# Performance work log

Measured on AMD Instinct MI355X. Metric: run time of the kernel, lower is better.

Reference implementation:

```python
import jax, jax.numpy as jnp
from jax import lax
import numpy as np

GRIDS = [40, 36, 24, 16, 12]
STRIDES = [4, 8, 16, 32, 64]
SCORE_THR = 0.3
MASK_THR = 0.5
UPDATE_THR = 0.05
SIGMA = 2.0
NMS_PRE = 500
MAX_PER_IMG = 30
E = 128            # ins_out_channels -> kernel_out_channels
HF = WF = 128      # seg feature map; upsampled_size_out = 4*HF = 512
IMG_H = IMG_W = 512
ORI_H = ORI_W = 512

# per-candidate stride, matching the cumsum-based fill in get_seg_single
STRIDE_PER_CELL = np.repeat(np.array(STRIDES, np.float32), [g * g for g in GRIDS])  # [3872]


def setup_inputs() -> dict:
    key = jax.random.key(0)
    ks = jax.random.split(key, 11)
    d = {}
    for i, g in enumerate(GRIDS):
        d[f"cate{i}"] = jax.random.uniform(ks[i], (1, g, g, 1), jnp.float32)
        d[f"kern{i}"] = jax.random.normal(ks[5 + i], (1, E, g, g), jnp.float32)
    d["seg_pred"] = jax.random.normal(ks[10], (1, E, HF, WF), jnp.float32)
    return d


def _forward_scores_and_masks(cates, kerns, seg_pred):
    # flatten all FPN levels, exactly mirroring view(-1,C)/permute(1,2,0).view(-1,E)
    scores = jnp.concatenate([c[0].reshape(-1) for c in cates])                 # [M]
    kernels = jnp.concatenate([k[0].transpose(1, 2, 0).reshape(-1, E) for k in kerns])  # [M,E]
    strides = jnp.asarray(STRIDE_PER_CELL)
    valid = scores > SCORE_THR                                                  # score_thr filter (as mask)

    # dynamic 1x1 conv over mask features == channel contraction
    seg_preds = jax.nn.sigmoid(jnp.einsum('me,ehw->mhw', kernels, seg_pred[0]))  # [M,HF,WF]
    seg_masks = seg_preds > MASK_THR
    sum_masks = seg_masks.sum((1, 2)).astype(jnp.float32)
    keep = valid & (sum_masks > strides)
    seg_scores = (seg_preds * seg_masks).sum((1, 2)) / jnp.maximum(sum_masks, 1.0)
    cscores = jnp.where(keep, scores * seg_scores, 0.0)

    # descending sort + truncate to nms_pre (dropped candidates carry score 0)
    top_scores, top_idx = lax.top_k(cscores, NMS_PRE)
    masks_k = seg_masks[top_idx].reshape(NMS_PRE, -1).astype(jnp.float32)       # [N,HW]
    sm = sum_masks[top_idx]

    # matrix NMS (single foreground class -> label matrix = triu of ones)
    inter = masks_k @ masks_k.T                                                 # [N,N]
    union = sm[None, :] + sm[:, None] - inter
    iou = jnp.triu(inter / jnp.maximum(union, 1.0), k=1)
    comp = iou.max(0)                              # max IoU with any higher-scored mask
    decay = jnp.exp(-SIGMA * (iou ** 2 - comp[:, None] ** 2))
    decay_coeff = decay.min(0)
    nms_scores = top_scores * decay_coeff
    nms_scores = jnp.where(nms_scores >= UPDATE_THR, nms_scores, 0.0)           # update_thr filter

    final_scores, fidx = lax.top_k(nms_scores, MAX_PER_IMG)
    sel = top_idx[fidx]
    sel_preds = seg_preds[sel]                                                  # [K,HF,WF]
    up = jax.image.resize(sel_preds, (MAX_PER_IMG, HF * 4, WF * 4), 'bilinear')  # align_corners=False
    up = up[:, :IMG_H, :IMG_W]
    up = jax.image.resize(up, (MAX_PER_IMG, ORI_H, ORI_W), 'bilinear')
    return final_scores, up


def reference(cate0, cate1, cate2, cate3, cate4,
              kern0, kern1, kern2, kern3, kern4, seg_pred):
    cates = [cate0, cate1, cate2, cate3, cate4]
    kerns = [kern0, kern1, kern2, kern3, kern4]
    final_scores, up = _forward_scores_and_masks(cates, kerns, seg_pred)
    seg_label = up > MASK_THR                                                   # [K,H,W]
    vis = final_scores > SCORE_THR                                              # vis_inds in forward()

    # masks_to_boxes, vectorized; invalid/empty rows zeroed (fixed-size output)
    any_x = seg_label.any(1)                                                    # [K,W]
    any_y = seg_label.any(2)                                                    # [K,H]
    xs = jnp.arange(ORI_W)
    ys = jnp.arange(ORI_H)
    xmin = jnp.min(jnp.where(any_x, xs, ORI_W), axis=1)
    xmax = jnp.max(jnp.where(any_x, xs, -1), axis=1)
    ymin = jnp.min(jnp.where(any_y, ys, ORI_H), axis=1)
    ymax = jnp.max(jnp.where(any_y, ys, -1), axis=1)
    boxes = jnp.stack([xmin, ymin, xmax, ymax], -1).astype(jnp.float32)         # [K,4]
    boxes = jnp.where(vis[:, None], boxes, 0.0)
    return boxes, final_scores, vis.astype(jnp.float32)
```

## Files before the change

kernel.cpp:

```cpp
#include <hip/hip_runtime.h>
#include <math.h>

#define M_CELLS 3872
#define M_PAD   3968
#define NPIX    16384

typedef _Float16 half8 __attribute__((ext_vector_type(8)));
typedef float f32x4 __attribute__((ext_vector_type(4)));

#define GL2LDS(g, l) __builtin_amdgcn_global_load_lds( \
    (const __attribute__((address_space(1))) unsigned int*)(g), \
    (__attribute__((address_space(3))) unsigned int*)(l), 16, 0, 0)

static constexpr size_t ALN(size_t x){ return (x + 255) & ~(size_t)255; }

static constexpr size_t F_KF   = 0;
static constexpr size_t F_SC   = F_KF + (size_t)M_CELLS*128*4;
static constexpr size_t F_SM   = F_SC + (size_t)M_CELLS*4;
static constexpr size_t F_CS   = F_SM + (size_t)M_CELLS*4;
static constexpr size_t F_BIT  = F_CS + (size_t)M_CELLS*4;
static constexpr size_t F_SPP  = F_BIT + (size_t)M_CELLS*256*8;
static constexpr size_t F_TIDX = F_SPP + (size_t)64*M_CELLS*4;
static constexpr size_t F_TSC  = F_TIDX + 512*4;
static constexpr size_t F_SMT  = F_TSC + 512*4;
static constexpr size_t F_IOU  = F_SMT + 512*4;
static constexpr size_t F_COMP = F_IOU + (size_t)500*500*4;
static constexpr size_t F_NMS  = F_COMP + 512*4;
static constexpr size_t F_SEL  = F_NMS + 512*4;
static constexpr size_t F_SELP = F_SEL + 32*4;
static constexpr size_t F_RMN  = ALN(F_SELP + (size_t)30*NPIX*4);
static constexpr size_t F_RMX  = F_RMN + 30*512*4;
static constexpr size_t F_KEYS = ALN(F_RMX + 30*512*4);
static constexpr size_t WS_FB  = F_KEYS + 4096*8;

static constexpr size_t B_KF   = 0;
static constexpr size_t B_AFR  = ALN(B_KF  + (size_t)M_PAD*128*4);
static constexpr size_t B_BFR  = ALN(B_AFR + (size_t)31*4096*16);
static constexpr size_t B_SC   = ALN(B_BFR + (size_t)128*4096*16);
static constexpr size_t B_SM   = ALN(B_SC + (size_t)M_PAD*4);
static constexpr size_t B_CS   = ALN(B_SM + (size_t)M_PAD*4);
static constexpr size_t B_BIT  = ALN(B_CS + (size_t)M_PAD*4);
static constexpr size_t B_SPP  = ALN(B_BIT + (size_t)M_PAD*256*8);
static constexpr size_t B_TIDX = ALN(B_SPP + (size_t)128*M_PAD*4);
static constexpr size_t B_TSC  = ALN(B_TIDX + 512*4);
static constexpr size_t B_SMT  = ALN(B_TSC + 512*4);
static constexpr size_t B_IOU  = ALN(B_SMT + 512*4);
static constexpr size_t B_COMP = ALN(B_IOU + (size_t)500*500*4);
static constexpr size_t B_NMS  = ALN(B_COMP + 512*4);
static constexpr size_t B_SEL  = ALN(B_NMS + 512*4);
static constexpr size_t B_SELP = ALN(B_SEL + 32*4);
static constexpr size_t B_RMN  = ALN(B_SELP + (size_t)30*NPIX*4);
static constexpr size_t B_RMX  = B_RMN + 30*512*4;
static constexpr size_t B_CMAP = ALN(B_RMX + 30*512*4);
static constexpr size_t B_RMAP = B_CMAP + 4096*4;
static constexpr size_t B_VCNT = B_RMAP + 4096*4;
static constexpr size_t B_KEYS = ALN(B_VCNT + 64*4);
static constexpr size_t B_AF30 = ALN(B_KEYS + 4096*8);
static constexpr size_t WS_MFMA = B_AF30 + 8*128*16;

__global__ __launch_bounds__(256) void k0aT_gather(
    const float* __restrict__ c0,const float* __restrict__ c1,const float* __restrict__ c2,
    const float* __restrict__ c3,const float* __restrict__ c4,
    const float* __restrict__ w0,const float* __restrict__ w1,const float* __restrict__ w2,
    const float* __restrict__ w3,const float* __restrict__ w4,
    float* __restrict__ kfT, float* __restrict__ scores,
    int* __restrict__ cmap, int* __restrict__ rmap, int* __restrict__ vcnt) {
  const int lvl = blockIdx.y;
  const int Gs[5]   = {1600,1296,576,256,144};
  const int offs[5] = {0,1600,2896,3472,3728};
  const int G = Gs[lvl], off = offs[lvl];
  const float* kl = (lvl==0)?w0:(lvl==1)?w1:(lvl==2)?w2:(lvl==3)?w3:w4;
  const float* cl = (lvl==0)?c0:(lvl==1)?c1:(lvl==2)?c2:(lvl==3)?c3:c4;
  int t = blockIdx.x*256 + threadIdx.x;
  if (t >= G*128) return;
  int e = t / G, c = t - e*G;
  kfT[(size_t)e*M_PAD + off + c] = kl[t];
  if (e == 0) {
    int cell = off + c;
    float sc = cl[c];
    scores[cell] = sc;
    if (sc > 0.3f) {
      int run = atomicAdd(vcnt, 1);
      cmap[run] = cell;
      rmap[cell] = run;
    } else rmap[cell] = -1;
  }
}

__global__ __launch_bounds__(256) void k0a_gather(
    const float* __restrict__ c0,const float* __restrict__ c1,const float* __restrict__ c2,
    const float* __restrict__ c3,const float* __restrict__ c4,
    const float* __restrict__ w0,const float* __restrict__ w1,const float* __restrict__ w2,
    const float* __restrict__ w3,const float* __restrict__ w4,
    float* __restrict__ kf, float* __restrict__ scores) {
  const int lvl = blockIdx.y;
  const int Gs[5]   = {1600,1296,576,256,144};
  const int offs[5] = {0,1600,2896,3472,3728};
  const int G = Gs[lvl], off = offs[lvl];
  const float* kl = (lvl==0)?w0:(lvl==1)?w1:(lvl==2)?w2:(lvl==3)?w3:w4;
  const float* cl = (lvl==0)?c0:(lvl==1)?c1:(lvl==2)?c2:(lvl==3)?c3:c4;
  int t = blockIdx.x*256 + threadIdx.x;
  if (t >= G*128) return;
  int e = t / G, c = t - e*G;
  kf[(size_t)(off+c)*128 + e] = kl[t];
  if (e == 0) scores[off+c] = cl[c];
}

__global__ __launch_bounds__(256) void k0b_afrag(const float* __restrict__ kfT,
                                                 const int* __restrict__ cmap,
                                                 const int* __restrict__ vcnt,
                                                 _Float16* __restrict__ Af) {
  int P = blockIdx.x*256 + threadIdx.x;
  int mblock = P >> 12;
  int r  = P & 4095;
  int sub = r >> 9, pc = r & 511;
  int ks = sub >> 1, h = sub & 1;
  int mn = pc >> 6, ln = pc & 63;
  int mcomp = mblock*128 + mn*16 + (ln & 15);
  int kb = ks*32 + (ln >> 4)*8;
  half8 o;
  if (mcomp < vcnt[0]) {
    const float* src = kfT + cmap[mcomp];
    #pragma unroll
    for (int j=0;j<8;j++) {
      float x = src[(size_t)(kb+j)*M_PAD];
      _Float16 hi = (_Float16)x;
      o[j] = h ? (_Float16)(x - (float)hi) : hi;
    }
  } else {
    #pragma unroll
    for (int j=0;j<8;j++) o[j] = (_Float16)0.f;
  }
  *(half8*)&Af[(size_t)P*8] = o;
}

__global__ __launch_bounds__(256) void k0c_bfrag(const float* __restrict__ seg,
                                                 _Float16* __restrict__ Bf) {
  int P = blockIdx.x*256 + threadIdx.x;
  int nb = P >> 12;
  int r  = P & 4095;
  int sub = r >> 9, pc = r & 511;
  int ks = sub >> 1, h = sub & 1;
  int mn = pc >> 6, ln = pc & 63;
  int px = nb*128 + mn*16 + (ln & 15);
  int kb = ks*32 + (ln >> 4)*8;
  half8 o;
  #pragma unroll
  for (int j=0;j<8;j++) {
    float x = seg[(size_t)(kb+j)*NPIX + px];
    _Float16 hi = (_Float16)x;
    o[j] = h ? (_Float16)(x - (float)hi) : hi;
  }
  *(half8*)&Bf[(size_t)P*8] = o;
}

__global__ __launch_bounds__(256, 6) void k1_gemm(
    const float* __restrict__ kf, const float* __restrict__ seg,
    unsigned long long* __restrict__ bits, float* __restrict__ spp) {
  int tid = threadIdx.x;
  int p  = blockIdx.x*256 + tid;
  int c0 = blockIdx.y*32;
  float acc[32];
  #pragma unroll
  for (int c=0;c<32;c++) acc[c]=0.f;
  for (int ch=0; ch<8; ch++) {
    float s[16];
    #pragma unroll
    for (int e=0;e<16;e++) s[e] = seg[(size_t)(ch*16+e)*NPIX + p];
    #pragma unroll
    for (int c=0;c<32;c++) {
      float a=0.f;
      #pragma unroll
      for (int e=0;e<16;e++) a = fmaf(kf[(size_t)(c0+c)*128 + ch*16 + e], s[e], a);
      acc[c] += a;
    }
  }
  int wv = tid>>6, ln = tid&63;
  __shared__ float wsum[32][4];
  #pragma unroll
  for (int c=0;c<32;c++) {
    float logit = acc[c];
    bool msk = logit > 0.f;
    unsigned long long bal = __ballot(msk);
    float pr = msk ? __fdividef(1.f, 1.f + __expf(-logit)) : 0.f;
    #pragma unroll
    for (int o=32;o>0;o>>=1) pr += __shfl_down(pr, o);
    if (ln==0) {
      bits[(size_t)(c0+c)*256 + blockIdx.x*4 + wv] = bal;
      wsum[c][wv] = pr;
    }
  }
  __syncthreads();
  if (tid < 32)
    spp[(size_t)blockIdx.x*M_CELLS + c0 + tid] = wsum[tid][0]+wsum[tid][1]+wsum[tid][2]+wsum[tid][3];
}

__global__ __launch_bounds__(256, 4) void k1_mfma(
    const _Float16* __restrict__ Af, const _Float16* __restrict__ Bf,
    const int* __restrict__ vcnt,
    unsigned long long* __restrict__ bits, float* __restrict__ spp) {
  if (blockIdx.x*128 >= vcnt[0]) return;
  __shared__ char lds[32768];
  const int tid  = threadIdx.x;
  const int lane = tid & 63;
  const int wave = tid >> 6;
  const int wr = wave >> 1, wc = wave & 1;
  const char* gA = (const char*)Af + (size_t)blockIdx.x*65536;
  const char* gB = (const char*)Bf + (size_t)blockIdx.y*65536;

  f32x4 acc[4][4];
  #pragma unroll
  for (int a=0;a<4;a++)
    #pragma unroll
    for (int b=0;b<4;b++) acc[a][b] = (f32x4){0.f,0.f,0.f,0.f};

  auto issue = [&](int sub, int buf) {
    const char* ga = gA + sub*8192;
    const char* gb = gB + sub*8192;
    char* la = &lds[buf*16384];
    char* lb = &lds[buf*16384 + 8192];
    GL2LDS(ga +  wave   *1024 + lane*16, la +  wave   *1024);
    GL2LDS(ga + (wave+4)*1024 + lane*16, la + (wave+4)*1024);
    GL2LDS(gb +  wave   *1024 + lane*16, lb +  wave   *1024);
    GL2LDS(gb + (wave+4)*1024 + lane*16, lb + (wave+4)*1024);
  };

  issue(0, 0);
  half8 ah[4], bh[4];
  #pragma unroll
  for (int s=0; s<8; s++) {
    __syncthreads();
    if (s < 7) issue(s+1, (s+1)&1);
    const char* lb_ = &lds[(s&1)*16384];
    if ((s & 1) == 0) {
      #pragma unroll
      for (int mt=0; mt<4; mt++) ah[mt] = *(const half8*)&lb_[(wr*4+mt)*1024 + lane*16];
      #pragma unroll
      for (int nt=0; nt<4; nt++) bh[nt] = *(const half8*)&lb_[8192 + (wc*4+nt)*1024 + lane*16];
      #pragma unroll
      for (int nt=0; nt<4; nt++)
        #pragma unroll
        for (int mt=0; mt<4; mt++)
          acc[mt][nt] = __builtin_amdgcn_mfma_f32_16x16x32_f16(ah[mt], bh[nt], acc[mt][nt], 0, 0, 0);
    } else {
      #pragma unroll
      for (int nt=0; nt<4; nt++) {
        half8 bl = *(const half8*)&lb_[8192 + (wc*4+nt)*1024 + lane*16];
        #pragma unroll
        for (int mt=0; mt<4; mt++)
          acc[mt][nt] = __builtin_amdgcn_mfma_f32_16x16x32_f16(ah[mt], bl, acc[mt][nt], 0, 0, 0);
      }
      #pragma unroll
      for (int mt=0; mt<4; mt++) {
        half8 al = *(const half8*)&lb_[(wr*4+mt)*1024 + lane*16];
        #pragma unroll
        for (int nt=0; nt<4; nt++)
          acc[mt][nt] = __builtin_amdgcn_mfma_f32_16x16x32_f16(al, bh[nt], acc[mt][nt], 0, 0, 0);
      }
    }
  }
  __syncthreads();

  const int q = lane >> 4, mm = lane & 15;
  const int mbase = blockIdx.x * 128;
  const int wordIdx = blockIdx.y*2 + wc;
  float* ldsf = (float*)lds;
  #pragma unroll
  for (int mt=0; mt<4; mt++) {
    #pragma unroll
    for (int reg=0; reg<4; reg++) {
      unsigned long long bal[4];
      float ps = 0.f;
      #pragma unroll
      for (int nt=0; nt<4; nt++) {
        float lg = acc[mt][nt][reg];
        bal[nt] = __ballot(lg > 0.f);
        if (lg > 0.f) ps += __fdividef(1.f, 1.f + __expf(-lg));
      }
      ps += __shfl_xor(ps, 1); ps += __shfl_xor(ps, 2);
      ps += __shfl_xor(ps, 4); ps += __shfl_xor(ps, 8);
      if (mm == 0) {
        int cl = wr*64 + mt*16 + q*4 + reg;
        unsigned long long wd = 0;
        #pragma unroll
        for (int nt=0; nt<4; nt++)
          wd |= ((bal[nt] >> (q*16)) & 0xFFFFull) << (nt*16);
        bits[(size_t)(mbase + cl)*256 + wordIdx] = wd;
        ldsf[cl*2 + wc] = ps;
      }
    }
  }
  __syncthreads();
  if (tid < 128)
    spp[(size_t)blockIdx.y*M_PAD + mbase + tid] = ldsf[tid*2] + ldsf[tid*2+1];
}

__global__ __launch_bounds__(256) void k2c_cscore(
    const unsigned long long* __restrict__ bits, const float* __restrict__ spp,
    const float* __restrict__ scores, const int* __restrict__ rmap,
    float* __restrict__ summ, float* __restrict__ cs) {
  int cell = blockIdx.x*4 + (threadIdx.x>>6);
  int ln = threadIdx.x & 63;
  int ridx = rmap[cell];
  if (ridx < 0) { if (ln==0) { summ[cell]=0.f; cs[cell]=0.f; } return; }
  const unsigned long long* row = bits + (size_t)ridx*256;
  int cnt = 0;
  #pragma unroll
  for (int k=0;k<4;k++) cnt += __popcll(row[ln + 64*k]);
  float sp = 0.f;
  for (int i=ln; i<128; i+=64) sp += spp[(size_t)i*M_PAD + ridx];
  #pragma unroll
  for (int o=32;o>0;o>>=1) { cnt += __shfl_down(cnt,o); sp += __shfl_down(sp,o); }
  if (ln==0) {
    float smf = (float)cnt;
    float sc = scores[cell];
    float strd = (cell<1600)?4.f:(cell<2896)?8.f:(cell<3472)?16.f:(cell<3728)?32.f:64.f;
    bool keep = (smf > strd);
    float ss = sp / fmaxf(smf, 1.f);
    summ[cell] = smf;
    cs[cell] = keep ? sc*ss : 0.f;
  }
}

__global__ __launch_bounds__(256) void k2_cscore(
    const unsigned long long* __restrict__ bits, const float* __restrict__ spp,
    const float* __restrict__ scores, float* __restrict__ summ, float* __restrict__ cs,
    int nparts, int mp) {
  int cell = blockIdx.x*4 + (threadIdx.x>>6);
  int ln = threadIdx.x & 63;
  const unsigned long long* row = bits + (size_t)cell*256;
  int cnt = 0;
  #pragma unroll
  for (int k=0;k<4;k++) cnt += __popcll(row[ln + 64*k]);
  float sp = 0.f;
  for (int i=ln; i<nparts; i+=64) sp += spp[(size_t)i*mp + cell];
  #pragma unroll
  for (int o=32;o>0;o>>=1) { cnt += __shfl_down(cnt,o); sp += __shfl_down(sp,o); }
  if (ln==0) {
    float smf = (float)cnt;
    float sc = scores[cell];
    float strd = (cell<1600)?4.f:(cell<2896)?8.f:(cell<3472)?16.f:(cell<3728)?32.f:64.f;
    bool keep = (sc > 0.3f) && (smf > strd);
    float ss = sp / fmaxf(smf, 1.f);
    summ[cell] = smf;
    cs[cell] = keep ? sc*ss : 0.f;
  }
}

__device__ inline unsigned long long packkey(float v, int i) {
  return ((unsigned long long)__float_as_uint(v) << 32) | (unsigned)(0xFFFFFFFFu - (unsigned)i);
}

__global__ __launch_bounds__(256) void k3a_sort512(const float* __restrict__ cs,
                                                   unsigned long long* __restrict__ keys) {
  __shared__ unsigned long long key[512];
  int b = blockIdx.x, tid = threadIdx.x;
  for (int i=tid;i<512;i+=256) {
    int gi = b*512 + i;
    key[i] = (gi < M_CELLS) ? packkey(cs[gi], gi) : 0ULL;
  }
  __syncthreads();
  for (int size=2; size<=512; size<<=1) {
    for (int st=size>>1; st>0; st>>=1) {
      for (int i=tid;i<512;i+=256) {
        int pp = i ^ st;
        if (pp > i) {
          unsigned long long a=key[i], bb=key[pp];
          bool desc = (((b*512+i) & size) == 0);
          if (desc ? (a<bb) : (a>bb)) { key[i]=bb; key[pp]=a; }
        }
      }
      __syncthreads();
    }
  }
  for (int i=tid;i<512;i+=256) keys[b*512+i] = key[i];
}

__global__ __launch_bounds__(1024) void k3b_merge(const unsigned long long* __restrict__ keys,
    const float* __restrict__ summ,
    int* __restrict__ tidx, float* __restrict__ tsc, float* __restrict__ smt) {
  __shared__ unsigned long long key[4096];
  int tid = threadIdx.x;
  for (int i=tid;i<4096;i+=1024) key[i] = keys[i];
  __syncthreads();
  for (int size=1024; size<=4096; size<<=1) {
    for (int st=size>>1; st>0; st>>=1) {
      for (int i=tid;i<4096;i+=1024) {
        int pp = i ^ st;
        if (pp > i) {
          unsigned long long a=key[i], b=key[pp];
          bool desc = ((i & size) == 0);
          if (desc ? (a<b) : (a>b)) { key[i]=b; key[pp]=a; }
        }
      }
      __syncthreads();
    }
  }
  if (tid < 512) {
    if (tid < 500) {
      unsigned long long k = key[tid];
      int idx = (int)(0xFFFFFFFFu - (unsigned)(k & 0xFFFFFFFFull));
      tidx[tid] = idx;
      tsc[tid] = __uint_as_float((unsigned)(k>>32));
      smt[tid] = summ[idx];
    } else { tidx[tid]=0; tsc[tid]=0.f; smt[tid]=0.f; }
  }
}

__global__ __launch_bounds__(256) void k4_iou(
    const unsigned long long* __restrict__ bits, const int* __restrict__ tidx,
    const int* __restrict__ rmap, const float* __restrict__ smt, float* __restrict__ iou) {
  int ti = blockIdx.y, tj = blockIdx.x;
  int tid = threadIdx.x;
  int ty = tid>>4, tx = tid&15;
  int i = ti*16+ty, j = tj*16+tx;
  if (ti > tj) { if (i<500 && j<500) iou[i*500+j] = 0.f; return; }
  __shared__ unsigned long long A[16][130];
  __shared__ unsigned long long B[16][130];
  __shared__ float sa[16], sb[16];
  if (tid<16) sa[tid] = (ti*16+tid<500) ? smt[ti*16+tid] : 0.f;
  else if (tid<32) sb[tid-16] = (tj*16+tid-16<500) ? smt[tj*16+tid-16] : 0.f;
  int inter = 0;
  for (int half=0; half<2; half++) {
    __syncthreads();
    for (int t=tid;t<2048;t+=256) {
      int r=t>>7, k=t&127;
      int ii = ti*16+r;
      int jj = tj*16+r;
      int ri = (ii<500) ? (rmap ? max(rmap[tidx[ii]],0) : tidx[ii]) : 0;
      int rj = (jj<500) ? (rmap ? max(rmap[tidx[jj]],0) : tidx[jj]) : 0;
      A[r][k] = (ii<500) ? bits[(size_t)ri*256 + half*128 + k] : 0ULL;
      B[r][k] = (jj<500) ? bits[(size_t)rj*256 + half*128 + k] : 0ULL;
    }
    __syncthreads();
    for (int k=0;k<128;k++) inter += __popcll(A[ty][k] & B[tx][k]);
  }
  if (i<500 && j<500) {
    float fi = (float)inter;
    float un = sa[ty] + sb[tx] - fi;
    iou[i*500+j] = (i<j) ? fi / fmaxf(un, 1.f) : 0.f;
  }
}

__global__ __launch_bounds__(256) void k5_comp(const float* __restrict__ iou, float* __restrict__ comp) {
  int tid = threadIdx.x;
  int tx = tid & 63, ty = tid >> 6;
  int j = blockIdx.x*64 + tx;
  float m0=0.f, m1=0.f, m2=0.f, m3=0.f;
  if (j < 500) {
    int i = ty;
    for (; i+12 < 500; i += 16) {
      m0 = fmaxf(m0, iou[(i   )*500 + j]);
      m1 = fmaxf(m1, iou[(i+ 4)*500 + j]);
      m2 = fmaxf(m2, iou[(i+ 8)*500 + j]);
      m3 = fmaxf(m3, iou[(i+12)*500 + j]);
    }
    for (; i < 500; i += 4) m0 = fmaxf(m0, iou[i*500 + j]);
  }
  float m = fmaxf(fmaxf(m0,m1), fmaxf(m2,m3));
  __shared__ float red[4][64];
  red[ty][tx] = m;
  __syncthreads();
  if (ty == 0 && j < 512)
    comp[j] = (j < 500) ? fmaxf(fmaxf(red[0][tx],red[1][tx]), fmaxf(red[2][tx],red[3][tx])) : 0.f;
}

__global__ __launch_bounds__(256) void k6_decay(
    const float* __restrict__ iou, const float* __restrict__ comp,
    const float* __restrict__ tsc, float* __restrict__ nms) {
  __shared__ float csh[512];
  int tid = threadIdx.x;
  for (int i=tid; i<512; i+=256) csh[i] = (i<500) ? comp[i] : 0.f;
  __syncthreads();
  int tx = tid & 63, ty = tid >> 6;
  int j = blockIdx.x*64 + tx;
  float t0=-1e30f, t1=-1e30f, t2=-1e30f, t3=-1e30f;
  if (j < 500) {
    int i = ty;
    for (; i+12 < 500; i += 16) {
      float v0 = iou[(i   )*500 + j], c0 = csh[i];
      float v1 = iou[(i+ 4)*500 + j], c1 = csh[i+4];
      float v2 = iou[(i+ 8)*500 + j], c2 = csh[i+8];
      float v3 = iou[(i+12)*500 + j], c3 = csh[i+12];
      t0 = fmaxf(t0, v0*v0 - c0*c0);
      t1 = fmaxf(t1, v1*v1 - c1*c1);
      t2 = fmaxf(t2, v2*v2 - c2*c2);
      t3 = fmaxf(t3, v3*v3 - c3*c3);
    }
    for (; i < 500; i += 4) { float v = iou[i*500 + j]; float c = csh[i]; t0 = fmaxf(t0, v*v - c*c); }
  }
  float t = fmaxf(fmaxf(t0,t1), fmaxf(t2,t3));
  __shared__ float red[4][64];
  red[ty][tx] = t;
  __syncthreads();
  if (ty == 0 && j < 512) {
    float out = 0.f;
    if (j < 500) {
      float tt = fmaxf(fmaxf(red[0][tx],red[1][tx]), fmaxf(red[2][tx],red[3][tx]));
      float s = tsc[j] * __expf(-2.f*tt);
      out = (s >= 0.05f) ? s : 0.f;
    }
    nms[j] = out;
  }
}

__global__ __launch_bounds__(256) void k7_top30(
    const float* __restrict__ nms, const int* __restrict__ tidx,
    int* __restrict__ sel, float* __restrict__ out,
    const float* __restrict__ kfT, _Float16* __restrict__ Af30) {
  __shared__ unsigned long long key[512];
  __shared__ int selsh[30];
  int tid = threadIdx.x;
  for (int i=tid;i<512;i+=256) key[i] = (i<500) ? packkey(nms[i], i) : 0ULL;
  __syncthreads();
  for (int size=2; size<=512; size<<=1) {
    for (int st=size>>1; st>0; st>>=1) {
      for (int i=tid;i<512;i+=256) {
        int pp = i ^ st;
        if (pp > i) {
          unsigned long long a=key[i], b=key[pp];
          bool desc = ((i & size) == 0);
          if (desc ? (a<b) : (a>b)) { key[i]=b; key[pp]=a; }
        }
      }
      __syncthreads();
    }
  }
  if (tid < 30) {
    unsigned long long k = key[tid];
    int j = (int)(0xFFFFFFFFu - (unsigned)(k & 0xFFFFFFFFull));
    float v = __uint_as_float((unsigned)(k>>32));
    out[120+tid] = v;
    out[150+tid] = (v > 0.3f) ? 1.f : 0.f;
    sel[tid] = tidx[j];
    selsh[tid] = tidx[j];
  }
  __syncthreads();
  if (kfT) {
    for (int P = tid; P < 1024; P += 256) {
      int sub = P >> 7, pc = P & 127;
      int ks = sub >> 1, h = sub & 1;
      int mn = pc >> 6, ln = pc & 63;
      int m  = mn*16 + (ln & 15);
      int kb = ks*32 + (ln >> 4)*8;
      half8 o;
      if (m < 30) {
        const float* src = kfT + selsh[m];
        #pragma unroll
        for (int j=0;j<8;j++) {
          float x = src[(size_t)(kb+j)*M_PAD];
          _Float16 hi = (_Float16)x;
          o[j] = h ? (_Float16)(x - (float)hi) : hi;
        }
      } else {
        #pragma unroll
        for (int j=0;j<8;j++) o[j] = (_Float16)0.f;
      }
      *(half8*)&Af30[(size_t)P*8] = o;
    }
  }
}

__global__ __launch_bounds__(256) void k8_mfma(const _Float16* __restrict__ Af30,
                                               const _Float16* __restrict__ Bf,
                                               float* __restrict__ selp) {
  const int nb = blockIdx.x;
  const int lane = threadIdx.x & 63;
  const int w = threadIdx.x >> 6;
  const half8* A = (const half8*)Af30;
  const half8* B = (const half8*)Bf + (size_t)nb*4096;
  f32x4 acc[2][2];
  #pragma unroll
  for (int a=0;a<2;a++)
    #pragma unroll
    for (int b=0;b<2;b++) acc[a][b] = (f32x4){0.f,0.f,0.f,0.f};
  #pragma unroll
  for (int ks=0; ks<4; ks++) {
    half8 ah[2], bh[2], al[2], bl[2];
    #pragma unroll
    for (int mt=0; mt<2; mt++) ah[mt] = A[(ks*2+0)*128 + mt*64 + lane];
    #pragma unroll
    for (int nt=0; nt<2; nt++) bh[nt] = B[(size_t)(ks*2+0)*512 + (w*2+nt)*64 + lane];
    #pragma unroll
    for (int mt=0; mt<2; mt++) al[mt] = A[(ks*2+1)*128 + mt*64 + lane];
    #pragma unroll
    for (int nt=0; nt<2; nt++) bl[nt] = B[(size_t)(ks*2+1)*512 + (w*2+nt)*64 + lane];
    #pragma unroll
    for (int nt=0; nt<2; nt++)
      #pragma unroll
      for (int mt=0; mt<2; mt++) {
        acc[mt][nt] = __builtin_amdgcn_mfma_f32_16x16x32_f16(ah[mt], bh[nt], acc[mt][nt], 0, 0, 0);
        acc[mt][nt] = __builtin_amdgcn_mfma_f32_16x16x32_f16(ah[mt], bl[nt], acc[mt][nt], 0, 0, 0);
        acc[mt][nt] = __builtin_amdgcn_mfma_f32_16x16x32_f16(al[mt], bh[nt], acc[mt][nt], 0, 0, 0);
      }
  }
  const int q = lane >> 4, col = lane & 15;
  #pragma unroll
  for (int mt=0; mt<2; mt++)
    #pragma unroll
    for (int nt=0; nt<2; nt++)
      #pragma unroll
      for (int reg=0; reg<4; reg++) {
        int m = mt*16 + q*4 + reg;
        if (m < 30) {
          int px = nb*128 + w*32 + nt*16 + col;
          float lg = acc[mt][nt][reg];
          selp[(size_t)m*NPIX + px] = __fdividef(1.f, 1.f + __expf(-lg));
        }
      }
}

__global__ __launch_bounds__(256) void k8_selp(
    const float* __restrict__ kf, const float* __restrict__ seg,
    const int* __restrict__ sel, float* __restrict__ selp) {
  int px = blockIdx.x*256 + threadIdx.x;
  int cells[30];
  #pragma unroll
  for (int m=0;m<30;m++) cells[m] = __builtin_amdgcn_readfirstlane(sel[m]);
  float acc[30];
  #pragma unroll
  for (int m=0;m<30;m++) acc[m] = 0.f;
  for (int e=0; e<128; e+=4) {
    float s0 = seg[(size_t)(e+0)*NPIX + px];
    float s1 = seg[(size_t)(e+1)*NPIX + px];
    float s2 = seg[(size_t)(e+2)*NPIX + px];
    float s3 = seg[(size_t)(e+3)*NPIX + px];
    #pragma unroll
    for (int m=0;m<30;m++) {
      const float* kr = kf + (size_t)cells[m]*128 + e;
      acc[m] = fmaf(kr[0], s0, fmaf(kr[1], s1, fmaf(kr[2], s2, fmaf(kr[3], s3, acc[m]))));
    }
  }
  #pragma unroll
  for (int m=0;m<30;m++)
    selp[(size_t)m*NPIX + px] = __fdividef(1.f, 1.f + __expf(-acc[m]));
}

__global__ __launch_bounds__(256) void k9a_rows(const float* __restrict__ selp,
                                               int* __restrict__ rowmn, int* __restrict__ rowmx) {
  int msk = blockIdx.y, oy = blockIdx.x;
  const float* mp = selp + (size_t)msk*NPIX;
  __shared__ float rows[2][128];
  __shared__ int wmn[4], wmx[4];
  int tid = threadIdx.x;
  float yf = fminf(fmaxf((oy+0.5f)*0.25f - 0.5f, 0.f), 127.f);
  int y0 = (int)yf, y1 = min(y0+1,127);
  float fy = yf-(float)y0;
  if (tid < 128) rows[0][tid] = mp[y0*128 + tid];
  else           rows[1][tid-128] = mp[y1*128 + tid-128];
  __syncthreads();
  int mnx = 512, mxx = -1;
  #pragma unroll
  for (int h=0; h<2; h++) {
    int ox = tid + h*256;
    float xf = fminf(fmaxf((ox+0.5f)*0.25f - 0.5f, 0.f), 127.f);
    int x0 = (int)xf, x1 = min(x0+1,127);
    float fx = xf-(float)x0;
    float v0 = rows[0][x0]*(1.f-fx) + rows[0][x1]*fx;
    float v1 = rows[1][x0]*(1.f-fx) + rows[1][x1]*fx;
    float v  = v0*(1.f-fy) + v1*fy;
    if (v > 0.5f) { mnx = min(mnx, ox); mxx = max(mxx, ox); }
  }
  #pragma unroll
  for (int o=32;o>0;o>>=1) {
    mnx = min(mnx, __shfl_down(mnx, o));
    mxx = max(mxx, __shfl_down(mxx, o));
  }
  if ((tid & 63) == 0) { wmn[tid>>6] = mnx; wmx[tid>>6] = mxx; }
  __syncthreads();
  if (tid == 0) {
    rowmn[msk*512 + oy] = min(min(wmn[0],wmn[1]), min(wmn[2],wmn[3]));
    rowmx[msk*512 + oy] = max(max(wmx[0],wmx[1]), max(wmx[2],wmx[3]));
  }
}

__global__ __launch_bounds__(512) void k9b_box(const int* __restrict__ rowmn,
                                              const int* __restrict__ rowmx, float* out) {
  int msk = blockIdx.x, tid = threadIdx.x;
  __shared__ int r0[512], r1[512], r2[512], r3[512];
  int mn = rowmn[msk*512 + tid];
  int mx = rowmx[msk*512 + tid];
  bool occ = (mx >= 0);
  r0[tid] = mn;
  r1[tid] = mx;
  r2[tid] = occ ? tid : 512;
  r3[tid] = occ ? tid : -1;
  __syncthreads();
  for (int s=256;s>0;s>>=1) {
    if (tid<s) {
      r0[tid]=min(r0[tid],r0[tid+s]); r1[tid]=max(r1[tid],r1[tid+s]);
      r2[tid]=min(r2[tid],r2[tid+s]); r3[tid]=max(r3[tid],r3[tid+s]);
    }
    __syncthreads();
  }
  if (tid==0) {
    bool vis = out[120+msk] > 0.3f;
    out[msk*4+0] = vis ? (float)r0[0] : 0.f;
    out[msk*4+1] = vis ? (float)r2[0] : 0.f;
    out[msk*4+2] = vis ? (float)r1[0] : 0.f;
    out[msk*4+3] = vis ? (float)r3[0] : 0.f;
  }
}

extern "C" void kernel_launch(void* const* d_in, const int* in_sizes, int n_in,
                              void* d_out, int out_size, void* d_ws, size_t ws_size,
                              hipStream_t stream) {
  (void)in_sizes; (void)n_in; (void)out_size;
  if (ws_size < WS_FB) return;
  const float* cate[5]; const float* kern[5];
  for (int i=0;i<5;i++){ cate[i]=(const float*)d_in[2*i]; kern[i]=(const float*)d_in[2*i+1]; }
  const float* seg = (const float*)d_in[10];
  char* ws = (char*)d_ws;
  float* out = (float*)d_out;

  const bool mfma = (ws_size >= WS_MFMA);

  float* kf      = (float*)(ws + (mfma ? B_KF   : F_KF));
  float* scores  = (float*)(ws + (mfma ? B_SC   : F_SC));
  float* summ    = (float*)(ws + (mfma ? B_SM   : F_SM));
  float* cs      = (float*)(ws + (mfma ? B_CS   : F_CS));
  unsigned long long* bits = (unsigned long long*)(ws + (mfma ? B_BIT : F_BIT));
  float* spp     = (float*)(ws + (mfma ? B_SPP  : F_SPP));
  int*   tidx    = (int*)(ws + (mfma ? B_TIDX : F_TIDX));
  float* tsc     = (float*)(ws + (mfma ? B_TSC  : F_TSC));
  float* smt     = (float*)(ws + (mfma ? B_SMT  : F_SMT));
  float* iou     = (float*)(ws + (mfma ? B_IOU  : F_IOU));
  float* comp    = (float*)(ws + (mfma ? B_COMP : F_COMP));
  float* nms     = (float*)(ws + (mfma ? B_NMS  : F_NMS));
  int*   sel     = (int*)(ws + (mfma ? B_SEL  : F_SEL));
  float* selp    = (float*)(ws + (mfma ? B_SELP : F_SELP));
  int*   rowmn   = (int*)(ws + (mfma ? B_RMN  : F_RMN));
  int*   rowmx   = (int*)(ws + (mfma ? B_RMX  : F_RMX));
  unsigned long long* keys = (unsigned long long*)(ws + (mfma ? B_KEYS : F_KEYS));

  if (mfma) {
    _Float16* Af = (_Float16*)(ws + B_AFR);
    _Float16* Bf = (_Float16*)(ws + B_BFR);
    _Float16* Af30 = (_Float16*)(ws + B_AF30);
    int* cmap = (int*)(ws + B_CMAP);
    int* rmap = (int*)(ws + B_RMAP);
    int* vcnt = (int*)(ws + B_VCNT);
    hipMemsetAsync(vcnt, 0, 4, stream);
    k0aT_gather<<<dim3(800,5), 256, 0, stream>>>(cate[0],cate[1],cate[2],cate[3],cate[4],
                                      kern[0],kern[1],kern[2],kern[3],kern[4],
                                      kf, scores, cmap, rmap, vcnt);
    k0c_bfrag<<<128*4096/256, 256, 0, stream>>>(seg, Bf);
    k0b_afrag<<<31*4096/256, 256, 0, stream>>>(kf, cmap, vcnt, Af);
    k1_mfma  <<<dim3(31, 128), 256, 0, stream>>>(Af, Bf, vcnt, bits, spp);
    k2c_cscore<<<M_CELLS/4, 256, 0, stream>>>(bits, spp, scores, rmap, summ, cs);
    k3a_sort512<<<8, 256, 0, stream>>>(cs, keys);
    k3b_merge  <<<1, 1024, 0, stream>>>(keys, summ, tidx, tsc, smt);
    k4_iou   <<<dim3(32,32), 256, 0, stream>>>(bits, tidx, rmap, smt, iou);
    k5_comp  <<<8, 256, 0, stream>>>(iou, comp);
    k6_decay <<<8, 256, 0, stream>>>(iou, comp, tsc, nms);
    k7_top30 <<<1, 256, 0, stream>>>(nms, tidx, sel, out, kf, Af30);
    k8_mfma  <<<128, 256, 0, stream>>>(Af30, Bf, selp);
  } else {
    k0a_gather<<<dim3(800,5), 256, 0, stream>>>(cate[0],cate[1],cate[2],cate[3],cate[4],
                                      kern[0],kern[1],kern[2],kern[3],kern[4], kf, scores);
    k1_gemm  <<<dim3(64,121), 256, 0, stream>>>(kf, seg, bits, spp);
    k2_cscore<<<M_CELLS/4, 256, 0, stream>>>(bits, spp, scores, summ, cs, 64, M_CELLS);
    k3a_sort512<<<8, 256, 0, stream>>>(cs, keys);
    k3b_merge  <<<1, 1024, 0, stream>>>(keys, summ, tidx, tsc, smt);
    k4_iou   <<<dim3(32,32), 256, 0, stream>>>(bits, tidx, nullptr, smt, iou);
    k5_comp  <<<8, 256, 0, stream>>>(iou, comp);
    k6_decay <<<8, 256, 0, stream>>>(iou, comp, tsc, nms);
    k7_top30 <<<1, 256, 0, stream>>>(nms, tidx, sel, out, nullptr, nullptr);
    k8_selp  <<<NPIX/256, 256, 0, stream>>>(kf, seg, sel, selp);
  }
  k9a_rows <<<dim3(512,30), 256, 0, stream>>>(selp, rowmn, rowmx);
  k9b_box  <<<30, 512, 0, stream>>>(rowmn, rowmx, out);
}
```

Measured before the change: 278.3 us.

## Merge small post-GEMM stages into cooperative kernels with grid-wide syncs

Replaces the cscore, two-pass sort and merge kernels with one cooperative kernel, the comp/decay/top30 kernels with a second, and the two bbox kernels with a third, each using grid.sync between phases. The aim is to cut kernel launch and inter-kernel gap overhead across a chain of tiny kernels. The cost is grid-wide barrier latency, and in coop_bbox some phases now run on a limited number of blocks, which lowers parallelism. Cooperative launch also requires every block to be co-resident on the device.

```diff
diff --git a/kernel.cpp b/kernel.cpp
--- a/kernel.cpp
+++ b/kernel.cpp
@@ -1,5 +1,8 @@
 #include <hip/hip_runtime.h>
+#include <hip/hip_cooperative_groups.h>
 #include <math.h>
+
+namespace cg = cooperative_groups;
 
 #define M_CELLS 3872
 #define M_PAD   3968
@@ -57,6 +60,10 @@
 static constexpr size_t B_KEYS = ALN(B_VCNT + 64*4);
 static constexpr size_t B_AF30 = ALN(B_KEYS + 4096*8);
 static constexpr size_t WS_MFMA = B_AF30 + 8*128*16;
+
+__device__ inline unsigned long long packkey(float v, int i) {
+  return ((unsigned long long)__float_as_uint(v) << 32) | (unsigned)(0xFFFFFFFFu - (unsigned)i);
+}
 
 __global__ __launch_bounds__(256) void k0aT_gather(
     const float* __restrict__ c0,const float* __restrict__ c1,const float* __restrict__ c2,
@@ -295,33 +302,6 @@
     spp[(size_t)blockIdx.y*M_PAD + mbase + tid] = ldsf[tid*2] + ldsf[tid*2+1];
 }
 
-__global__ __launch_bounds__(256) void k2c_cscore(
-    const unsigned long long* __restrict__ bits, const float* __restrict__ spp,
-    const float* __restrict__ scores, const int* __restrict__ rmap,
-    float* __restrict__ summ, float* __restrict__ cs) {
-  int cell = blockIdx.x*4 + (threadIdx.x>>6);
-  int ln = threadIdx.x & 63;
-  int ridx = rmap[cell];
-  if (ridx < 0) { if (ln==0) { summ[cell]=0.f; cs[cell]=0.f; } return; }
-  const unsigned long long* row = bits + (size_t)ridx*256;
-  int cnt = 0;
-  #pragma unroll
-  for (int k=0;k<4;k++) cnt += __popcll(row[ln + 64*k]);
-  float sp = 0.f;
-  for (int i=ln; i<128; i+=64) sp += spp[(size_t)i*M_PAD + ridx];
-  #pragma unroll
-  for (int o=32;o>0;o>>=1) { cnt += __shfl_down(cnt,o); sp += __shfl_down(sp,o); }
-  if (ln==0) {
-    float smf = (float)cnt;
-    float sc = scores[cell];
-    float strd = (cell<1600)?4.f:(cell<2896)?8.f:(cell<3472)?16.f:(cell<3728)?32.f:64.f;
-    bool keep = (smf > strd);
-    float ss = sp / fmaxf(smf, 1.f);
-    summ[cell] = smf;
-    cs[cell] = keep ? sc*ss : 0.f;
-  }
-}
-
 __global__ __launch_bounds__(256) void k2_cscore(
     const unsigned long long* __restrict__ bits, const float* __restrict__ spp,
     const float* __restrict__ scores, float* __restrict__ summ, float* __restrict__ cs,
@@ -347,8 +327,90 @@
   }
 }
 
-__device__ inline unsigned long long packkey(float v, int i) {
-  return ((unsigned long long)__float_as_uint(v) << 32) | (unsigned)(0xFFFFFFFFu - (unsigned)i);
+__global__ __launch_bounds__(1024) void coop_sort(
+    const unsigned long long* __restrict__ bits, const float* __restrict__ spp,
+    const float* __restrict__ scores, const int* __restrict__ rmap,
+    float* __restrict__ summ, float* __restrict__ cs,
+    unsigned long long* __restrict__ keys,
+    int* __restrict__ tidx, float* __restrict__ tsc, float* __restrict__ smt) {
+  cg::grid_group grid = cg::this_grid();
+  __shared__ unsigned long long key[4096];
+  int tid = threadIdx.x;
+  {
+    int cell = blockIdx.x*16 + (tid>>6);
+    int ln = tid & 63;
+    int ridx = rmap[cell];
+    if (ridx < 0) {
+      if (ln==0) { summ[cell]=0.f; cs[cell]=0.f; }
+    } else {
+      const unsigned long long* row = bits + (size_t)ridx*256;
+      int cnt = 0;
+      #pragma unroll
+      for (int k=0;k<4;k++) cnt += __popcll(row[ln + 64*k]);
+      float sp = spp[(size_t)ln*M_PAD + ridx] + spp[(size_t)(ln+64)*M_PAD + ridx];
+      #pragma unroll
+      for (int o=32;o>0;o>>=1) { cnt += __shfl_down(cnt,o); sp += __shfl_down(sp,o); }
+      if (ln==0) {
+        float smf = (float)cnt;
+        float sc = scores[cell];
+        float strd = (cell<1600)?4.f:(cell<2896)?8.f:(cell<3472)?16.f:(cell<3728)?32.f:64.f;
+        bool keep = (smf > strd);
+        float ss = sp / fmaxf(smf, 1.f);
+        summ[cell] = smf;
+        cs[cell] = keep ? sc*ss : 0.f;
+      }
+    }
+  }
+  grid.sync();
+  if (blockIdx.x < 8) {
+    int b = blockIdx.x;
+    if (tid < 512) {
+      int gi = b*512 + tid;
+      key[tid] = (gi < M_CELLS) ? packkey(cs[gi], gi) : 0ULL;
+    }
+    __syncthreads();
+    for (int size=2; size<=512; size<<=1) {
+      for (int st=size>>1; st>0; st>>=1) {
+        if (tid < 512) {
+          int i = tid, pp = i ^ st;
+          if (pp > i) {
+            unsigned long long a=key[i], bb=key[pp];
+            bool desc = (((b*512+i) & size) == 0);
+            if (desc ? (a<bb) : (a>bb)) { key[i]=bb; key[pp]=a; }
+          }
+        }
+        __syncthreads();
+      }
+    }
+    if (tid < 512) keys[b*512+tid] = key[tid];
+  }
+  grid.sync();
+  if (blockIdx.x == 0) {
+    for (int i=tid;i<4096;i+=1024) key[i] = keys[i];
+    __syncthreads();
+    for (int size=1024; size<=4096; size<<=1) {
+      for (int st=size>>1; st>0; st>>=1) {
+        for (int i=tid;i<4096;i+=1024) {
+          int pp = i ^ st;
+          if (pp > i) {
+            unsigned long long a=key[i], b=key[pp];
+            bool desc = ((i & size) == 0);
+            if (desc ? (a<b) : (a>b)) { key[i]=b; key[pp]=a; }
+          }
+        }
+        __syncthreads();
+      }
+    }
+    if (tid < 512) {
+      if (tid < 500) {
+        unsigned long long k = key[tid];
+        int idx = (int)(0xFFFFFFFFu - (unsigned)(k & 0xFFFFFFFFull));
+        tidx[tid] = idx;
+        tsc[tid] = __uint_as_float((unsigned)(k>>32));
+        smt[tid] = summ[idx];
+      } else { tidx[tid]=0; tsc[tid]=0.f; smt[tid]=0.f; }
+    }
+  }
 }
 
 __global__ __launch_bounds__(256) void k3a_sort512(const float* __restrict__ cs,
@@ -439,6 +501,122 @@
     float fi = (float)inter;
     float un = sa[ty] + sb[tx] - fi;
     iou[i*500+j] = (i<j) ? fi / fmaxf(un, 1.f) : 0.f;
+  }
+}
+
+__global__ __launch_bounds__(256) void coop_nms(
+    const float* __restrict__ iou, const float* __restrict__ tsc,
+    const int* __restrict__ tidx, float* __restrict__ comp,
+    float* __restrict__ nms, int* __restrict__ sel, float* __restrict__ out,
+    const float* __restrict__ kfT, _Float16* __restrict__ Af30) {
+  cg::grid_group grid = cg::this_grid();
+  __shared__ float red[4][64];
+  __shared__ float csh[512];
+  __shared__ unsigned long long key[512];
+  __shared__ int selsh[30];
+  int tid = threadIdx.x;
+  int tx = tid & 63, ty = tid >> 6;
+  {
+    int j = blockIdx.x*64 + tx;
+    float m0=0.f, m1=0.f, m2=0.f, m3=0.f;
+    if (j < 500) {
+      int i = ty;
+      for (; i+12 < 500; i += 16) {
+        m0 = fmaxf(m0, iou[(i   )*500 + j]);
+        m1 = fmaxf(m1, iou[(i+ 4)*500 + j]);
+        m2 = fmaxf(m2, iou[(i+ 8)*500 + j]);
+        m3 = fmaxf(m3, iou[(i+12)*500 + j]);
+      }
+      for (; i < 500; i += 4) m0 = fmaxf(m0, iou[i*500 + j]);
+    }
+    float m = fmaxf(fmaxf(m0,m1), fmaxf(m2,m3));
+    red[ty][tx] = m;
+    __syncthreads();
+    if (ty == 0 && j < 512)
+      comp[j] = (j < 500) ? fmaxf(fmaxf(red[0][tx],red[1][tx]), fmaxf(red[2][tx],red[3][tx])) : 0.f;
+  }
+  grid.sync();
+  {
+    for (int i=tid; i<512; i+=256) csh[i] = (i<500) ? comp[i] : 0.f;
+    __syncthreads();
+    int j = blockIdx.x*64 + tx;
+    float t0=-1e30f, t1=-1e30f, t2=-1e30f, t3=-1e30f;
+    if (j < 500) {
+      int i = ty;
+      for (; i+12 < 500; i += 16) {
+        float v0 = iou[(i   )*500 + j], c0 = csh[i];
+        float v1 = iou[(i+ 4)*500 + j], c1 = csh[i+4];
+        float v2 = iou[(i+ 8)*500 + j], c2 = csh[i+8];
+        float v3 = iou[(i+12)*500 + j], c3 = csh[i+12];
+        t0 = fmaxf(t0, v0*v0 - c0*c0);
+        t1 = fmaxf(t1, v1*v1 - c1*c1);
+        t2 = fmaxf(t2, v2*v2 - c2*c2);
+        t3 = fmaxf(t3, v3*v3 - c3*c3);
+      }
+      for (; i < 500; i += 4) { float v = iou[i*500 + j]; float c = csh[i]; t0 = fmaxf(t0, v*v - c*c); }
+    }
+    float t = fmaxf(fmaxf(t0,t1), fmaxf(t2,t3));
+    __syncthreads();
+    red[ty][tx] = t;
+    __syncthreads();
+    if (ty == 0 && j < 512) {
+      float o = 0.f;
+      if (j < 500) {
+        float tt = fmaxf(fmaxf(red[0][tx],red[1][tx]), fmaxf(red[2][tx],red[3][tx]));
+        float s = tsc[j] * __expf(-2.f*tt);
+        o = (s >= 0.05f) ? s : 0.f;
+      }
+      nms[j] = o;
+    }
+  }
+  grid.sync();
+  if (blockIdx.x == 0) {
+    for (int i=tid;i<512;i+=256) key[i] = (i<500) ? packkey(nms[i], i) : 0ULL;
+    __syncthreads();
+    for (int size=2; size<=512; size<<=1) {
+      for (int st=size>>1; st>0; st>>=1) {
+        for (int i=tid;i<512;i+=256) {
+          int pp = i ^ st;
+          if (pp > i) {
+            unsigned long long a=key[i], b=key[pp];
+            bool desc = ((i & size) == 0);
+            if (desc ? (a<b) : (a>b)) { key[i]=b; key[pp]=a; }
+          }
+        }
+        __syncthreads();
+      }
+    }
+    if (tid < 30) {
+      unsigned long long k = key[tid];
+      int j = (int)(0xFFFFFFFFu - (unsigned)(k & 0xFFFFFFFFull));
+      float v = __uint_as_float((unsigned)(k>>32));
+      out[120+tid] = v;
+      out[150+tid] = (v > 0.3f) ? 1.f : 0.f;
+      sel[tid] = tidx[j];
+      selsh[tid] = tidx[j];
+    }
+    __syncthreads();
+    for (int P = tid; P < 1024; P += 256) {
+      int sub = P >> 7, pc = P & 127;
+      int ks = sub >> 1, h = sub & 1;
+      int mn = pc >> 6, ln = pc & 63;
+      int m  = mn*16 + (ln & 15);
+      int kb = ks*32 + (ln >> 4)*8;
+      half8 o;
+      if (m < 30) {
+        const float* src = kfT + selsh[m];
+        #pragma unroll
+        for (int j=0;j<8;j++) {
+          float x = src[(size_t)(kb+j)*M_PAD];
+          _Float16 hi = (_Float16)x;
+          o[j] = h ? (_Float16)(x - (float)hi) : hi;
+        }
+      } else {
+        #pragma unroll
+        for (int j=0;j<8;j++) o[j] = (_Float16)0.f;
+      }
+      *(half8*)&Af30[(size_t)P*8] = o;
+    }
   }
 }
 
@@ -636,6 +814,75 @@
     selp[(size_t)m*NPIX + px] = __fdividef(1.f, 1.f + __expf(-acc[m]));
 }
 
+__global__ __launch_bounds__(256) void coop_bbox(const float* __restrict__ selp,
+    int* __restrict__ rowmn, int* __restrict__ rowmx, float* __restrict__ out) {
+  cg::grid_group grid = cg::this_grid();
+  __shared__ float rows[2][128];
+  __shared__ int wmn[4], wmx[4];
+  __shared__ int r0[256], r1[256], r2[256], r3[256];
+  int tid = threadIdx.x;
+  for (int it=0; it<30; it++) {
+    int u = it*512 + blockIdx.x;
+    int msk = u >> 9, oy = u & 511;
+    const float* mp = selp + (size_t)msk*NPIX;
+    float yf = fminf(fmaxf((oy+0.5f)*0.25f - 0.5f, 0.f), 127.f);
+    int y0 = (int)yf, y1 = min(y0+1,127);
+    float fy = yf-(float)y0;
+    if (tid < 128) rows[0][tid] = mp[y0*128 + tid];
+    else           rows[1][tid-128] = mp[y1*128 + tid-128];
+    __syncthreads();
+    int mnx = 512, mxx = -1;
+    #pragma unroll
+    for (int h=0; h<2; h++) {
+      int ox = tid + h*256;
+      float xf = fminf(fmaxf((ox+0.5f)*0.25f - 0.5f, 0.f), 127.f);
+      int x0 = (int)xf, x1 = min(x0+1,127);
+      float fx = xf-(float)x0;
+      float v0 = rows[0][x0]*(1.f-fx) + rows[0][x1]*fx;
+      float v1 = rows[1][x0]*(1.f-fx) + rows[1][x1]*fx;
+      float v  = v0*(1.f-fy) + v1*fy;
+      if (v > 0.5f) { mnx = min(mnx, ox); mxx = max(mxx, ox); }
+    }
+    #pragma unroll
+    for (int o=32;o>0;o>>=1) {
+      mnx = min(mnx, __shfl_down(mnx, o));
+      mxx = max(mxx, __shfl_down(mxx, o));
+    }
+    if ((tid & 63) == 0) { wmn[tid>>6] = mnx; wmx[tid>>6] = mxx; }
+    __syncthreads();
+    if (tid == 0) {
+      rowmn[msk*512 + oy] = min(min(wmn[0],wmn[1]), min(wmn[2],wmn[3]));
+      rowmx[msk*512 + oy] = max(max(wmx[0],wmx[1]), max(wmx[2],wmx[3]));
+    }
+    __syncthreads();
+  }
+  grid.sync();
+  if (blockIdx.x < 30) {
+    int msk = blockIdx.x;
+    int mn0 = rowmn[msk*512 + tid],       mx0 = rowmx[msk*512 + tid];
+    int mn1 = rowmn[msk*512 + tid + 256], mx1 = rowmx[msk*512 + tid + 256];
+    r0[tid] = min(mn0, mn1);
+    r1[tid] = max(mx0, mx1);
+    r2[tid] = min((mx0>=0)?tid:512, (mx1>=0)?(tid+256):512);
+    r3[tid] = max((mx0>=0)?tid:-1,  (mx1>=0)?(tid+256):-1);
+    __syncthreads();
+    for (int s=128;s>0;s>>=1) {
+      if (tid<s) {
+        r0[tid]=min(r0[tid],r0[tid+s]); r1[tid]=max(r1[tid],r1[tid+s]);
+        r2[tid]=min(r2[tid],r2[tid+s]); r3[tid]=max(r3[tid],r3[tid+s]);
+      }
+      __syncthreads();
+    }
+    if (tid==0) {
+      bool vis = out[120+msk] > 0.3f;
+      out[msk*4+0] = vis ? (float)r0[0] : 0.f;
+      out[msk*4+1] = vis ? (float)r2[0] : 0.f;
+      out[msk*4+2] = vis ? (float)r1[0] : 0.f;
+      out[msk*4+3] = vis ? (float)r3[0] : 0.f;
+    }
+  }
+}
+
 __global__ __launch_bounds__(256) void k9a_rows(const float* __restrict__ selp,
                                                int* __restrict__ rowmn, int* __restrict__ rowmx) {
   int msk = blockIdx.y, oy = blockIdx.x;
@@ -747,14 +994,27 @@
     k0c_bfrag<<<128*4096/256, 256, 0, stream>>>(seg, Bf);
     k0b_afrag<<<31*4096/256, 256, 0, stream>>>(kf, cmap, vcnt, Af);
     k1_mfma  <<<dim3(31, 128), 256, 0, stream>>>(Af, Bf, vcnt, bits, spp);
-    k2c_cscore<<<M_CELLS/4, 256, 0, stream>>>(bits, spp, scores, rmap, summ, cs);
-    k3a_sort512<<<8, 256, 0, stream>>>(cs, keys);
-    k3b_merge  <<<1, 1024, 0, stream>>>(keys, summ, tidx, tsc, smt);
+    {
+      const unsigned long long* bitsc = bits;
+      const float* sppc = spp; const float* scoresc = scores; const int* rmapc = rmap;
+      void* p[] = { (void*)&bitsc, (void*)&sppc, (void*)&scoresc, (void*)&rmapc,
+                    (void*)&summ, (void*)&cs, (void*)&keys, (void*)&tidx, (void*)&tsc, (void*)&smt };
+      hipLaunchCooperativeKernel((const void*)coop_sort, dim3(242), dim3(1024), p, 0, stream);
+    }
     k4_iou   <<<dim3(32,32), 256, 0, stream>>>(bits, tidx, rmap, smt, iou);
-    k5_comp  <<<8, 256, 0, stream>>>(iou, comp);
-    k6_decay <<<8, 256, 0, stream>>>(iou, comp, tsc, nms);
-    k7_top30 <<<1, 256, 0, stream>>>(nms, tidx, sel, out, kf, Af30);
+    {
+      const float* iouc = iou; const float* tscc = tsc; const int* tidxc = tidx;
+      const float* kfc = kf;
+      void* p[] = { (void*)&iouc, (void*)&tscc, (void*)&tidxc, (void*)&comp,
+                    (void*)&nms, (void*)&sel, (void*)&out, (void*)&kfc, (void*)&Af30 };
+      hipLaunchCooperativeKernel((const void*)coop_nms, dim3(8), dim3(256), p, 0, stream);
+    }
     k8_mfma  <<<128, 256, 0, stream>>>(Af30, Bf, selp);
+    {
+      const float* selpc = selp;
+      void* p[] = { (void*)&selpc, (void*)&rowmn, (void*)&rowmx, (void*)&out };
+      hipLaunchCooperativeKernel((const void*)coop_bbox, dim3(512), dim3(256), p, 0, stream);
+    }
   } else {
     k0a_gather<<<dim3(800,5), 256, 0, stream>>>(cate[0],cate[1],cate[2],cate[3],cate[4],
                                       kern[0],kern[1],kern[2],kern[3],kern[4], kf, scores);
@@ -767,7 +1027,7 @@
     k6_decay <<<8, 256, 0, stream>>>(iou, comp, tsc, nms);
     k7_top30 <<<1, 256, 0, stream>>>(nms, tidx, sel, out, nullptr, nullptr);
     k8_selp  <<<NPIX/256, 256, 0, stream>>>(kf, seg, sel, selp);
-  }
-  k9a_rows <<<dim3(512,30), 256, 0, stream>>>(selp, rowmn, rowmx);
-  k9b_box  <<<30, 512, 0, stream>>>(rowmn, rowmx, out);
-}
+    k9a_rows <<<dim3(512,30), 256, 0, stream>>>(selp, rowmn, rowmx);
+    k9b_box  <<<30, 512, 0, stream>>>(rowmn, rowmx, out);
+  }
+}
```

New measurement: 434.6 us. 56.2% more time.
